# Optimization experiments

Hardware: AMD Instinct MI355X
Metric: run time of the kernel (lower is better)

Reference implementation:

```python
import jax, jax.numpy as jnp
import numpy as np

V, H, HP, HOUT, G = 500_000, 128, 128, 128, 25_000


def setup_inputs() -> dict:
    key = jax.random.key(0)
    ks = jax.random.split(key, 7)
    node_features = jax.random.normal(ks[0], (V, H), dtype=jnp.float32)
    s = jnp.float32(1.0 / np.sqrt(H))
    W_up = jax.random.normal(ks[1], (H, HP), dtype=jnp.float32) * s
    b_up = jax.random.normal(ks[2], (HP,), dtype=jnp.float32) * jnp.float32(0.02)
    W_gate = jax.random.normal(ks[3], (H, HP), dtype=jnp.float32) * s
    b_gate = jax.random.normal(ks[4], (HP,), dtype=jnp.float32) * jnp.float32(0.02)
    W_func = jax.random.normal(ks[5], (HP, HOUT), dtype=jnp.float32) * s
    b_func = jax.random.normal(ks[6], (HOUT,), dtype=jnp.float32) * jnp.float32(0.02)
    # graph offsets: G graphs, each with >=2 nodes, summing exactly to V (sorted, last = V)
    rng = np.random.default_rng(0)
    sizes = rng.multinomial(V - 2 * G, np.full(G, 1.0 / G)) + 2
    starts = np.concatenate([[0], np.cumsum(sizes)]).astype(np.int64)
    assert starts[-1] == V
    node_grp_start_with_end = jnp.asarray(starts)
    max_size = int(sizes.max())
    return {
        "node_features": node_features,
        "W_up": W_up, "b_up": b_up,
        "W_gate": W_gate, "b_gate": b_gate,
        "W_func": W_func, "b_func": b_func,
        "node_grp_start_with_end": node_grp_start_with_end,
        "max_size": max_size,
    }


def reference(node_features, W_up, b_up, W_gate, b_gate, W_func, b_func,
              node_grp_start_with_end, max_size):
    starts = node_grp_start_with_end  # [g+1], sorted, starts[-1] == v
    g = starts.shape[0] - 1
    v = node_features.shape[0]

    proj_up = node_features @ W_up + b_up            # [v, hp]
    gate = jax.nn.sigmoid(node_features @ W_gate + b_gate)
    gated = gate * proj_up                            # [v, hp]

    # segment id of each node: graph i where starts[i] <= n < starts[i+1]
    n = jnp.arange(v)
    seg = jnp.searchsorted(starts, n, side="right") - 1  # [v]

    # faithful to original loop: end = next_start - 1, so the LAST node of each
    # graph is EXCLUDED from the padded copy (and hence from the sum)
    keep = n != (starts[seg + 1] - 1)                 # [v] bool

    graph_sums = jax.ops.segment_sum(
        jnp.where(keep[:, None], gated, jnp.float32(0.0)), seg, num_segments=g
    )                                                 # [g, hp]

    return graph_sums @ W_func + b_func               # [g, h_out]
```

## Files before the change

### kernel.cpp

```cpp
#include <hip/hip_runtime.h>


typedef __bf16 bf16_t;
typedef bf16_t bf16x8 __attribute__((ext_vector_type(8)));
typedef float  f32x4  __attribute__((ext_vector_type(4)));

#define XS_STRIDE 144
#define GS_STRIDE 132

__device__ __forceinline__ unsigned short f2bf(float f) {
  unsigned int u = __float_as_uint(f);
  u += 0x7fffu + ((u >> 16) & 1u);
  return (unsigned short)(u >> 16);
}

__device__ __forceinline__ void bar_lds() {
  asm volatile("s_waitcnt lgkmcnt(0)\n\ts_barrier" ::: "memory");
}

__global__ void tile_seg_kernel(const int* __restrict__ starts,
                                int* __restrict__ tile_seg,
                                int ntiles, int G) {
  int i = blockIdx.x * blockDim.x + threadIdx.x;
  if (i >= ntiles) return;
  int n0 = i * 64;
  int lo = 0, hi = G - 1;
  while (lo < hi) {
    int mid = (lo + hi + 1) >> 1;
    if (starts[mid] <= n0) lo = mid; else hi = mid - 1;
  }
  tile_seg[i] = lo;
}

__global__ __launch_bounds__(256, 3)
void stage1_kernel(const float* __restrict__ X,
                   const float* __restrict__ Wu, const float* __restrict__ bu,
                   const float* __restrict__ Wg, const float* __restrict__ bg,
                   const int* __restrict__ starts,
                   const int* __restrict__ tile_seg,
                   float* __restrict__ gsum, int V, int G, int ntiles)
{
  __shared__ unsigned short Xs[64 * XS_STRIDE];
  __shared__ float          Gs[64 * GS_STRIDE];

  const int tid  = threadIdx.x;
  const int lane = tid & 63;
  const int wave = tid >> 6;
  const int quad = lane >> 4;
  const int l15  = lane & 15;

  bf16x8 Bu[2][4], Bg[2][4];
  float bup[2], bgt[2];
#pragma unroll
  for (int t = 0; t < 2; ++t) {
    const int f = wave * 32 + t * 16 + l15;
    bup[t] = bu[f];
    bgt[t] = bg[f];
#pragma unroll
    for (int s = 0; s < 4; ++s) {
      const int k0 = s * 32 + quad * 8;
      union { unsigned short us[8]; bf16x8 v; } a, b;
#pragma unroll
      for (int j = 0; j < 8; ++j) {
        a.us[j] = f2bf(Wu[(k0 + j) * 128 + f]);
        b.us[j] = f2bf(Wg[(k0 + j) * 128 + f]);
      }
      Bu[t][s] = a.v;
      Bg[t][s] = b.v;
    }
  }

  f32x4 ld[8];
  int tile = blockIdx.x;

  int g0v, sval;
  {
    const int t0 = min(tile, ntiles - 1);
    g0v  = tile_seg[t0];
    sval = starts[min(g0v + lane, G)];
    const int n0 = t0 * 64;
#pragma unroll
    for (int i = 0; i < 8; ++i) {
      const int flat = tid + i * 256;
      const int n = min(n0 + (flat >> 5), V - 1);
      const int k = (flat & 31) << 2;
      ld[i] = *(const f32x4*)(X + (size_t)n * 128 + k);
    }
  }

  for (; tile < ntiles; tile += gridDim.x) {
    const int n0    = tile * 64;
    const int n_end = min(n0 + 64, V);
    const int g0 = g0v;
    const int sv = sval;

#pragma unroll
    for (int i = 0; i < 8; ++i) {
      const int flat = tid + i * 256;
      const int n = flat >> 5;
      const int k = (flat & 31) << 2;
      const unsigned int p0 =
          (unsigned int)f2bf(ld[i][0]) | ((unsigned int)f2bf(ld[i][1]) << 16);
      const unsigned int p1 =
          (unsigned int)f2bf(ld[i][2]) | ((unsigned int)f2bf(ld[i][3]) << 16);
      *(uint2*)&Xs[n * XS_STRIDE + k] = make_uint2(p0, p1);
    }

    const int nextc = min(tile + (int)gridDim.x, ntiles - 1);
    {
      const int m0 = nextc * 64;
#pragma unroll
      for (int i = 0; i < 8; ++i) {
        const int flat = tid + i * 256;
        const int n = min(m0 + (flat >> 5), V - 1);
        const int k = (flat & 31) << 2;
        ld[i] = *(const f32x4*)(X + (size_t)n * 128 + k);
      }
    }
    g0v  = tile_seg[nextc];
    sval = starts[min(g0v + lane, G)];

    bar_lds();

#pragma unroll
    for (int sub = 0; sub < 4; ++sub) {
      bf16x8 A[4];
      const int nl = sub * 16 + l15;
#pragma unroll
      for (int s = 0; s < 4; ++s)
        A[s] = *(const bf16x8*)&Xs[nl * XS_STRIDE + s * 32 + quad * 8];
#pragma unroll
      for (int t = 0; t < 2; ++t) {
        f32x4 au = {0.f, 0.f, 0.f, 0.f};
        f32x4 ag = {0.f, 0.f, 0.f, 0.f};
#pragma unroll
        for (int s = 0; s < 4; ++s) {
          au = __builtin_amdgcn_mfma_f32_16x16x32_bf16(A[s], Bu[t][s], au, 0, 0, 0);
          ag = __builtin_amdgcn_mfma_f32_16x16x32_bf16(A[s], Bg[t][s], ag, 0, 0, 0);
        }
        const int f = wave * 32 + t * 16 + l15;
#pragma unroll
        for (int r = 0; r < 4; ++r) {
          const float up = au[r] + bup[t];
          const float gt = ag[r] + bgt[t];
          const float gv = up * __builtin_amdgcn_rcpf(1.f + __expf(-gt));
          Gs[(sub * 16 + quad * 4 + r) * GS_STRIDE + f] = gv;
        }
      }
    }

    bar_lds();

    {
      const int fcol = tid & 127;
      const int half = tid >> 7;
      int i = 0;
      int sg = __shfl(sv, 0);
      while (sg < n_end && i < 63) {
        const int snext = __shfl(sv, i + 1);
        if (((g0 + i) & 1) == half) {
          const int r0 = max(sg, n0) - n0;
          const int r1 = min(snext - 1, n_end) - n0;
          if (r1 > r0) {
            float a0 = 0.f, a1 = 0.f, a2 = 0.f, a3 = 0.f;
            int r = r0;
            for (; r + 4 <= r1; r += 4) {
              a0 += Gs[(r + 0) * GS_STRIDE + fcol];
              a1 += Gs[(r + 1) * GS_STRIDE + fcol];
              a2 += Gs[(r + 2) * GS_STRIDE + fcol];
              a3 += Gs[(r + 3) * GS_STRIDE + fcol];
            }
            for (; r < r1; ++r) a0 += Gs[r * GS_STRIDE + fcol];
            const float acc = (a0 + a1) + (a2 + a3);
            atomicAdd(&gsum[(size_t)(g0 + i) * 128 + fcol], acc);
          }
        }
        sg = snext;
        ++i;
      }
    }
  }
}

__global__ __launch_bounds__(256)
void stage2_kernel(const float* __restrict__ Wf, const float* __restrict__ bfv,
                   float* __restrict__ out, int G)
{
  __shared__ float Gsm[32 * 132];
  const int g0  = blockIdx.x * 32;
  const int tid = threadIdx.x;

  for (int i = tid; i < 32 * 32; i += 256) {
    const int r = i >> 5;
    const int c = (i & 31) << 2;
    const int g = g0 + r;
    f32x4 v = {0.f, 0.f, 0.f, 0.f};
    if (g < G) v = *(const f32x4*)(out + (size_t)g * 128 + c);
    *(f32x4*)&Gsm[r * 132 + c] = v;
  }
  __syncthreads();

  const int fq  = tid & 31;
  const int f0  = fq << 2;
  const int grp = tid >> 5;
  float acc[4][4];
#pragma unroll
  for (int i = 0; i < 4; ++i)
#pragma unroll
    for (int j = 0; j < 4; ++j) acc[i][j] = 0.f;

#pragma unroll 4
  for (int k = 0; k < 128; ++k) {
    const f32x4 w = *(const f32x4*)(Wf + (size_t)k * 128 + f0);
#pragma unroll
    for (int i = 0; i < 4; ++i) {
      const float gv = Gsm[(grp * 4 + i) * 132 + k];
      acc[i][0] += gv * w[0];
      acc[i][1] += gv * w[1];
      acc[i][2] += gv * w[2];
      acc[i][3] += gv * w[3];
    }
  }

  const f32x4 bb = *(const f32x4*)(bfv + f0);
#pragma unroll
  for (int i = 0; i < 4; ++i) {
    const int g = g0 + grp * 4 + i;
    if (g < G) {
      f32x4 o = {acc[i][0] + bb[0], acc[i][1] + bb[1],
                 acc[i][2] + bb[2], acc[i][3] + bb[3]};
      *(f32x4*)(out + (size_t)g * 128 + f0) = o;
    }
  }
}

extern "C" void kernel_launch(void* const* d_in, const int* in_sizes, int n_in,
                              void* d_out, int out_size, void* d_ws, size_t ws_size,
                              hipStream_t stream)
{
  const float* X      = (const float*)d_in[0];
  const float* Wu     = (const float*)d_in[1];
  const float* bu     = (const float*)d_in[2];
  const float* Wg     = (const float*)d_in[3];
  const float* bg     = (const float*)d_in[4];
  const float* Wf     = (const float*)d_in[5];
  const float* bf_    = (const float*)d_in[6];
  const int*   starts = (const int*)d_in[7];

  const int G = in_sizes[7] - 1;
  const int V = in_sizes[0] / 128;
  const int ntiles = (V + 63) / 64;

  int*   tile_seg = (int*)d_ws;
  float* gsum     = (float*)d_out;

  hipMemsetAsync(d_out, 0, (size_t)G * 128 * sizeof(float), stream);
  tile_seg_kernel<<<(ntiles + 255) / 256, 256, 0, stream>>>(starts, tile_seg, ntiles, G);
  stage1_kernel<<<768, 256, 0, stream>>>(X, Wu, bu, Wg, bg, starts, tile_seg,
                                         gsum, V, G, ntiles);
  stage2_kernel<<<(G + 31) / 32, 256, 0, stream>>>(Wf, bf_, gsum, G);
}
```

Measured before the change: 404.0 us.

## Reduce gated rows in registers with cross-lane shuffles and double-buffer X tile

Gated values now stay in registers instead of being written to an LDS staging buffer. Per-graph row sums are computed by masked accumulation over each lane's 16 rows, followed by xor-shuffles across quads, so one LDS round-trip and one barrier per tile are removed. The X tile in LDS is double-buffered so the next tile's writes do not race with the current tile's reads once that barrier is gone. The cost is that every segment now loops over all 16 rows per lane plus four shuffles, and the register array may raise register pressure.

```diff
diff --git a/kernel.cpp b/kernel.cpp
--- a/kernel.cpp
+++ b/kernel.cpp
@@ -6,7 +6,6 @@
 typedef float  f32x4  __attribute__((ext_vector_type(4)));
 
 #define XS_STRIDE 144
-#define GS_STRIDE 132
 
 __device__ __forceinline__ unsigned short f2bf(float f) {
   unsigned int u = __float_as_uint(f);
@@ -40,8 +39,7 @@
                    const int* __restrict__ tile_seg,
                    float* __restrict__ gsum, int V, int G, int ntiles)
 {
-  __shared__ unsigned short Xs[64 * XS_STRIDE];
-  __shared__ float          Gs[64 * GS_STRIDE];
+  __shared__ unsigned short Xs[2][64 * XS_STRIDE];
 
   const int tid  = threadIdx.x;
   const int lane = tid & 63;
@@ -88,11 +86,13 @@
     }
   }
 
-  for (; tile < ntiles; tile += gridDim.x) {
+  int it = 0;
+  for (; tile < ntiles; tile += gridDim.x, ++it) {
     const int n0    = tile * 64;
     const int n_end = min(n0 + 64, V);
     const int g0 = g0v;
     const int sv = sval;
+    unsigned short* xb = Xs[it & 1];
 
 #pragma unroll
     for (int i = 0; i < 8; ++i) {
@@ -103,7 +103,7 @@
           (unsigned int)f2bf(ld[i][0]) | ((unsigned int)f2bf(ld[i][1]) << 16);
       const unsigned int p1 =
           (unsigned int)f2bf(ld[i][2]) | ((unsigned int)f2bf(ld[i][3]) << 16);
-      *(uint2*)&Xs[n * XS_STRIDE + k] = make_uint2(p0, p1);
+      *(uint2*)&xb[n * XS_STRIDE + k] = make_uint2(p0, p1);
     }
 
     const int nextc = min(tile + (int)gridDim.x, ntiles - 1);
@@ -122,13 +122,14 @@
 
     bar_lds();
 
+    float gv[4][2][4];
 #pragma unroll
     for (int sub = 0; sub < 4; ++sub) {
       bf16x8 A[4];
       const int nl = sub * 16 + l15;
 #pragma unroll
       for (int s = 0; s < 4; ++s)
-        A[s] = *(const bf16x8*)&Xs[nl * XS_STRIDE + s * 32 + quad * 8];
+        A[s] = *(const bf16x8*)&xb[nl * XS_STRIDE + s * 32 + quad * 8];
 #pragma unroll
       for (int t = 0; t < 2; ++t) {
         f32x4 au = {0.f, 0.f, 0.f, 0.f};
@@ -138,42 +139,40 @@
           au = __builtin_amdgcn_mfma_f32_16x16x32_bf16(A[s], Bu[t][s], au, 0, 0, 0);
           ag = __builtin_amdgcn_mfma_f32_16x16x32_bf16(A[s], Bg[t][s], ag, 0, 0, 0);
         }
-        const int f = wave * 32 + t * 16 + l15;
 #pragma unroll
         for (int r = 0; r < 4; ++r) {
           const float up = au[r] + bup[t];
           const float gt = ag[r] + bgt[t];
-          const float gv = up * __builtin_amdgcn_rcpf(1.f + __expf(-gt));
-          Gs[(sub * 16 + quad * 4 + r) * GS_STRIDE + f] = gv;
+          gv[sub][t][r] = up * __builtin_amdgcn_rcpf(1.f + __expf(-gt));
         }
       }
     }
 
-    bar_lds();
-
     {
-      const int fcol = tid & 127;
-      const int half = tid >> 7;
       int i = 0;
       int sg = __shfl(sv, 0);
       while (sg < n_end && i < 63) {
         const int snext = __shfl(sv, i + 1);
-        if (((g0 + i) & 1) == half) {
-          const int r0 = max(sg, n0) - n0;
-          const int r1 = min(snext - 1, n_end) - n0;
-          if (r1 > r0) {
-            float a0 = 0.f, a1 = 0.f, a2 = 0.f, a3 = 0.f;
-            int r = r0;
-            for (; r + 4 <= r1; r += 4) {
-              a0 += Gs[(r + 0) * GS_STRIDE + fcol];
-              a1 += Gs[(r + 1) * GS_STRIDE + fcol];
-              a2 += Gs[(r + 2) * GS_STRIDE + fcol];
-              a3 += Gs[(r + 3) * GS_STRIDE + fcol];
+        const int r0 = max(sg, n0) - n0;
+        const int r1 = min(snext - 1, n_end) - n0;
+        if (r1 > r0) {
+          float p0 = 0.f, p1 = 0.f;
+#pragma unroll
+          for (int sub = 0; sub < 4; ++sub) {
+#pragma unroll
+            for (int r = 0; r < 4; ++r) {
+              const int row = sub * 16 + quad * 4 + r;
+              const bool in = (row >= r0) && (row < r1);
+              p0 += in ? gv[sub][0][r] : 0.f;
+              p1 += in ? gv[sub][1][r] : 0.f;
             }
-            for (; r < r1; ++r) a0 += Gs[r * GS_STRIDE + fcol];
-            const float acc = (a0 + a1) + (a2 + a3);
-            atomicAdd(&gsum[(size_t)(g0 + i) * 128 + fcol], acc);
           }
+          p0 += __shfl_xor(p0, 16); p0 += __shfl_xor(p0, 32);
+          p1 += __shfl_xor(p1, 16); p1 += __shfl_xor(p1, 32);
+          if (quad == 0)
+            atomicAdd(&gsum[(size_t)(g0 + i) * 128 + wave * 32 + l15], p0);
+          else if (quad == 1)
+            atomicAdd(&gsum[(size_t)(g0 + i) * 128 + wave * 32 + 16 + l15], p1);
         }
         sg = snext;
         ++i;
```

After: 510.3 us. 26.3% more time.
